# Kernel tuning notes

Hardware: AMD Instinct MI355X
Metric: run time of the kernel (lower is better)

Reference implementation:

```python
import jax, jax.numpy as jnp
import numpy as np

N, C, H, E = 4096, 512, 8, 131072
D = C // H
ALPHA = 0.5
EPS = 1e-5


def layer_norm(x, g, b):
    mu = jnp.mean(x, axis=-1, keepdims=True)
    var = jnp.mean((x - mu) ** 2, axis=-1, keepdims=True)
    return (x - mu) * jax.lax.rsqrt(var + EPS) * g + b


def setup_inputs() -> dict:
    key = jax.random.key(0)
    ks = jax.random.split(key, 20)
    s = 0.02
    return {
        "x": jax.random.normal(ks[0], (N, C), jnp.float32),
        "edge_index": jax.random.randint(ks[1], (2, E), 0, N, jnp.int32),
        "local_w": jax.random.normal(ks[2], (C, C), jnp.float32) * s,
        "local_b": jnp.zeros((C,), jnp.float32),
        "in_proj_w": jax.random.normal(ks[3], (3 * C, C), jnp.float32) * s,
        "in_proj_b": jnp.zeros((3 * C,), jnp.float32),
        "attn_out_w": jax.random.normal(ks[4], (C, C), jnp.float32) * s,
        "attn_out_b": jnp.zeros((C,), jnp.float32),
        "output_w": jax.random.normal(ks[5], (C, C), jnp.float32) * s,
        "output_b": jnp.zeros((C,), jnp.float32),
        "norm1_g": jnp.ones((C,), jnp.float32),
        "norm1_b": jnp.zeros((C,), jnp.float32),
        "norm2_g": jnp.ones((C,), jnp.float32),
        "norm2_b": jnp.zeros((C,), jnp.float32),
        "ffn_w1": jax.random.normal(ks[6], (2 * C, C), jnp.float32) * s,
        "ffn_b1": jnp.zeros((2 * C,), jnp.float32),
        "ffn_w2": jax.random.normal(ks[7], (C, 2 * C), jnp.float32) * s,
        "ffn_b2": jnp.zeros((C,), jnp.float32),
    }


def reference(x, edge_index, local_w, local_b, in_proj_w, in_proj_b,
              attn_out_w, attn_out_b, output_w, output_b,
              norm1_g, norm1_b, norm2_g, norm2_b,
              ffn_w1, ffn_b1, ffn_w2, ffn_b2):
    src, dst = edge_index[0], edge_index[1]

    # local branch: linear then scatter-mean over incoming edges
    local_h = x @ local_w.T + local_b                       # [N,C]
    summed = jax.ops.segment_sum(local_h[src], dst, num_segments=N)
    cnt = jax.ops.segment_sum(jnp.ones((E,), x.dtype), dst, num_segments=N)
    local_out = summed / jnp.maximum(cnt, 1.0)[:, None]

    # global branch: full self-attention over all nodes
    qkv = x @ in_proj_w.T + in_proj_b                       # [N,3C]
    q, k, v = jnp.split(qkv, 3, axis=-1)
    q = q.reshape(N, H, D)
    k = k.reshape(N, H, D)
    v = v.reshape(N, H, D)
    scores = jnp.einsum('nhd,mhd->hnm', q, k) / jnp.sqrt(jnp.asarray(D, x.dtype))
    attn = jax.nn.softmax(scores, axis=-1)                  # [H,N,N]
    ctx = jnp.einsum('hnm,mhd->nhd', attn, v).reshape(N, C)
    global_out = ctx @ attn_out_w.T + attn_out_b

    mixed = ALPHA * local_out + (1.0 - ALPHA) * global_out
    hidden = layer_norm(x + (mixed @ output_w.T + output_b), norm1_g, norm1_b)

    ff = jax.nn.gelu(hidden @ ffn_w1.T + ffn_b1, approximate=False) @ ffn_w2.T + ffn_b2
    return layer_norm(hidden + ff, norm2_g, norm2_b)
```

## Files before the change

kernel.cpp:

```cpp
#include <hip/hip_runtime.h>


#define N_NODES 4096
#define C_DIM   512
#define H_HEADS 8
#define D_HEAD  64
#define E_EDGES 131072

typedef unsigned short u16;
typedef unsigned int   u32;
typedef u16   u16x8  __attribute__((ext_vector_type(8)));
typedef __bf16 bf16x8 __attribute__((ext_vector_type(8)));
typedef float  f32x4  __attribute__((ext_vector_type(4)));
typedef u32    u32x4  __attribute__((ext_vector_type(4)));

__device__ __forceinline__ float b2f(u16 u) {
  unsigned int i = ((unsigned int)u) << 16;
  return __builtin_bit_cast(float, i);
}
__device__ __forceinline__ u16 f2b(float f) {
  unsigned int i = __builtin_bit_cast(unsigned int, f);
  i += 0x7fffu + ((i >> 16) & 1u);
  return (u16)(i >> 16);
}
__device__ __forceinline__ u32 cvtpk(float lo, float hi) {
  u32 r;
  asm("v_cvt_pk_bf16_f32 %0, %1, %2" : "=v"(r) : "v"(lo), "v"(hi));
  return r;
}
__device__ __forceinline__ void pl32swap(u32& x, u32& y) {
  asm("v_permlane32_swap_b32 %0, %1" : "+v"(x), "+v"(y));
}
__device__ __forceinline__ void pl16swap(u32& x, u32& y) {
  asm("v_permlane16_swap_b32 %0, %1" : "+v"(x), "+v"(y));
}
__device__ __forceinline__ void glds16(const u16* g, u16* l) {
  __builtin_amdgcn_global_load_lds(
      (const __attribute__((address_space(1))) void*)g,
      (__attribute__((address_space(3))) void*)l, 16, 0, 0);
}

struct CvtArgs {
  const float* src[7];
  u16* dst[7];
  int n[7];
  int* deg;
};

__global__ __launch_bounds__(256) void cvt_multi(CvtArgs a) {
  const int t = blockIdx.y;
  if (t == 7) {
    const int i = blockIdx.x * 256 + threadIdx.x;
    if (i < N_NODES) a.deg[i] = 0;
    return;
  }
  const int i = (blockIdx.x * 256 + threadIdx.x) * 8;
  if (i >= a.n[t]) return;
  const float* s = a.src[t] + i;
  f32x4 v0 = *(const f32x4*)s;
  f32x4 v1 = *(const f32x4*)(s + 4);
  u16x8 o;
  o[0]=f2b(v0[0]); o[1]=f2b(v0[1]); o[2]=f2b(v0[2]); o[3]=f2b(v0[3]);
  o[4]=f2b(v1[0]); o[5]=f2b(v1[1]); o[6]=f2b(v1[2]); o[7]=f2b(v1[3]);
  *(u16x8*)(a.dst[t] + i) = o;
}

template<int EPI>
__global__ __launch_bounds__(256) void gemm_bt(
    const u16* __restrict__ A, const u16* __restrict__ W,
    const float* __restrict__ bias, void* __restrict__ outp,
    int M, int Nout, int K,
    const float* __restrict__ mloc)
{
  const int tid  = threadIdx.x;
  const int lane = tid & 63, wave = tid >> 6;
  const int quad = lane >> 4, l16 = lane & 15;
  const int wm = wave >> 1, wn = wave & 1;
  const int bm = blockIdx.x, bnb = blockIdx.y;

  __shared__ __align__(16) u16 As[64][128];
  __shared__ __align__(16) u16 Ws[64][128];

  f32x4 acc[2][2] = {};

  const int lr4 = lane >> 4, gs = lane & 15;
  const int g8e = (gs ^ lr4) * 8;
  const int g8o = (gs ^ (4 + lr4)) * 8;
  const u16* aw[8];
#pragma unroll
  for (int c = 0; c < 4; ++c) {
    const int g8 = (c & 1) ? g8o : g8e;
    aw[c]     = A + (size_t)(bm  * 64 + wave * 16 + c * 4 + lr4) * K + g8;
    aw[4 + c] = W + (size_t)(bnb * 64 + wave * 16 + c * 4 + lr4) * K + g8;
  }

  for (int k0 = 0; k0 < K; k0 += 128) {
    __syncthreads();
#pragma unroll
    for (int c = 0; c < 4; ++c) {
      glds16(aw[c] + k0,     &As[wave * 16 + c * 4][0]);
      glds16(aw[4 + c] + k0, &Ws[wave * 16 + c * 4][0]);
    }
    __syncthreads();
#pragma unroll
    for (int ks = 0; ks < 4; ++ks) {
      const int slot = ((ks * 4 + quad) ^ (l16 & 7)) * 8;
      bf16x8 af[2], bf[2];
      af[0] = *(const bf16x8*)&As[wm * 32 +      l16][slot];
      af[1] = *(const bf16x8*)&As[wm * 32 + 16 + l16][slot];
      bf[0] = *(const bf16x8*)&Ws[wn * 32 +      l16][slot];
      bf[1] = *(const bf16x8*)&Ws[wn * 32 + 16 + l16][slot];
#pragma unroll
      for (int i = 0; i < 2; ++i)
#pragma unroll
        for (int j = 0; j < 2; ++j)
          acc[i][j] = __builtin_amdgcn_mfma_f32_16x16x32_bf16(af[i], bf[j], acc[i][j], 0, 0, 0);
    }
  }

#pragma unroll
  for (int i = 0; i < 2; ++i)
#pragma unroll
    for (int j = 0; j < 2; ++j) {
      const int col = bnb * 64 + wn * 32 + j * 16 + l16;
      const float bias_v = bias[col];
#pragma unroll
      for (int r = 0; r < 4; ++r) {
        const int row = bm * 64 + wm * 32 + i * 16 + quad * 4 + r;
        float v = acc[i][j][r] + bias_v;
        const size_t o = (size_t)row * Nout + col;
        if constexpr (EPI == 1) {
          ((float*)outp)[o] = v;
        } else if constexpr (EPI == 2) {
          float gl = 0.5f * v * (1.0f + erff(v * 0.70710678118654752f));
          ((u16*)outp)[o] = f2b(gl);
        } else {
          ((u16*)outp)[o] = f2b(0.5f * mloc[o] + 0.5f * v);
        }
      }
    }
}

__global__ __launch_bounds__(256) void gemm128(
    const u16* __restrict__ A, const u16* __restrict__ W,
    const float* __restrict__ bias0, const float* __restrict__ bias1,
    u16* __restrict__ out0, u16* __restrict__ out1,
    int M, int Nout, int K,
    const int* __restrict__ ei, int* __restrict__ deg)
{
  const int tid  = threadIdx.x;
  if (blockIdx.y == 16) {
#pragma unroll
    for (int i = 0; i < 16; ++i) {
      const int e = blockIdx.x * 4096 + i * 256 + tid;
      atomicAdd(&deg[ei[E_EDGES + e]], 1);
    }
    return;
  }
  const int lane = tid & 63, wave = tid >> 6;
  const int quad = lane >> 4, l16 = lane & 15;
  const int wm = wave >> 1, wn = wave & 1;
  const int bm = blockIdx.x, bnb = blockIdx.y;

  __shared__ __align__(16) u16 As[128][64];
  __shared__ __align__(16) u16 Ws[128][64];

  f32x4 acc[4][4] = {};

  const int lr = lane >> 3, gs = lane & 7;
  const int g8 = (gs ^ lr) * 8;
  const u16* ab = A + (size_t)(bm  * 128 + wave * 32 + lr) * K + g8;
  const u16* wb = W + (size_t)(bnb * 128 + wave * 32 + lr) * K + g8;

  for (int k0 = 0; k0 < K; k0 += 64) {
    __syncthreads();
#pragma unroll
    for (int c = 0; c < 4; ++c) {
      glds16(ab + (size_t)(c * 8) * K + k0, &As[wave * 32 + c * 8][0]);
      glds16(wb + (size_t)(c * 8) * K + k0, &Ws[wave * 32 + c * 8][0]);
    }
    __syncthreads();
#pragma unroll
    for (int ks = 0; ks < 2; ++ks) {
      const int slot = ((ks * 4 + quad) ^ (l16 & 7)) * 8;
      bf16x8 af[4], bf[4];
#pragma unroll
      for (int am = 0; am < 4; ++am)
        af[am] = *(const bf16x8*)&As[wm * 64 + am * 16 + l16][slot];
#pragma unroll
      for (int bn = 0; bn < 4; ++bn)
        bf[bn] = *(const bf16x8*)&Ws[wn * 64 + bn * 16 + l16][slot];
#pragma unroll
      for (int am = 0; am < 4; ++am)
#pragma unroll
        for (int bn = 0; bn < 4; ++bn)
          acc[am][bn] = __builtin_amdgcn_mfma_f32_16x16x32_bf16(af[am], bf[bn], acc[am][bn], 0, 0, 0);
    }
  }

#pragma unroll
  for (int am = 0; am < 4; ++am)
#pragma unroll
    for (int bn = 0; bn < 4; ++bn) {
      const int col = bnb * 128 + wn * 64 + bn * 16 + l16;
      const float bias_v = (col < 512) ? bias0[col] : bias1[col - 512];
#pragma unroll
      for (int r = 0; r < 4; ++r) {
        const int row = bm * 128 + wm * 64 + am * 16 + quad * 4 + r;
        float v = acc[am][bn][r] + bias_v;
        if (col < 512) out0[(size_t)row * 512 + col] = f2b(v);
        else           out1[(size_t)row * 1536 + (col - 512)] = f2b(v);
      }
    }
}

__global__ __launch_bounds__(256) void scan_vtrans(
    const int* __restrict__ deg, int* __restrict__ off, int* __restrict__ cursor,
    const u16* __restrict__ qkv, u16* __restrict__ vt)
{
  if (blockIdx.x == 512) {
    __shared__ int part[256];
    const int t = threadIdx.x;
    int v[16];
    int s = 0;
#pragma unroll
    for (int i = 0; i < 16; ++i) { v[i] = deg[t * 16 + i]; s += v[i]; }
    part[t] = s;
    __syncthreads();
    for (int d = 1; d < 256; d <<= 1) {
      int val = (t >= d) ? part[t - d] : 0;
      __syncthreads();
      if (t >= d) part[t] += val;
      __syncthreads();
    }
    int prefix = (t == 0) ? 0 : part[t - 1];
#pragma unroll
    for (int i = 0; i < 16; ++i) {
      off[t * 16 + i] = prefix;
      cursor[t * 16 + i] = prefix;
      prefix += v[i];
    }
    if (t == 255) off[4096] = prefix;
    return;
  }
  __shared__ __align__(16) u16 T[64][64];
  const int tid = threadIdx.x;
  const int h = blockIdx.x >> 6, mt = blockIdx.x & 63;
  const int m0 = mt * 64;
  const int c  = tid & 7;
  const int mr = tid >> 3;
#pragma unroll
  for (int half = 0; half < 2; ++half) {
    const int m = mr + half * 32;
    const u16x8 v = *(const u16x8*)(qkv + (size_t)(m0 + m) * 1536 + 1024 + h * 64 + c * 8);
    *(u16x8*)&T[m][((c ^ (m >> 3)) * 8)] = v;
  }
  __syncthreads();
#pragma unroll
  for (int half = 0; half < 2; ++half) {
    const int q = tid + half * 256;
    const int d = q >> 3, mc = q & 7;
    u16x8 w;
#pragma unroll
    for (int e = 0; e < 8; ++e)
      w[e] = T[mc * 8 + e][(((d >> 3) ^ mc) * 8) + (d & 7)];
    *(u16x8*)(vt + (size_t)(h * 64 + d) * N_NODES + m0 + mc * 8) = w;
  }
}

template<int SPLITS>
__global__ __launch_bounds__(256) void attn_kernel(
    const u16* __restrict__ qkv, const u16* __restrict__ vt,
    u16* __restrict__ opart, float* __restrict__ lpart,
    const int* __restrict__ ei, int* __restrict__ cursor, int* __restrict__ csr)
{
  const int tid = threadIdx.x, wave = tid >> 6, lane = tid & 63;
  const int split = blockIdx.z;
  if (split == SPLITS) {
    const int sblk = blockIdx.y * 32 + blockIdx.x;
#pragma unroll
    for (int i = 0; i < 2; ++i) {
      const int e = sblk * 512 + i * 256 + tid;
      const int s = ei[e];
      const int d = ei[E_EDGES + e];
      const int p = atomicAdd(&cursor[d], 1);
      csr[p] = s;
    }
    return;
  }
  const int quad = lane >> 4, l16 = lane & 15;
  const int h = blockIdx.x & 7;
  const int tile = (blockIdx.x >> 3) + (blockIdx.y << 2);

  __shared__ __align__(16) u16 Ks[2][64][64];
  __shared__ __align__(16) u16 Vts[2][64][64];

  const float QSCALE = 0.18033688011112042f;
  bf16x8 aq[2][2];
#pragma unroll
  for (int mb = 0; mb < 2; ++mb) {
    const int qrow = tile * 128 + wave * 32 + mb * 16 + l16;
    const u16* qp = qkv + (size_t)qrow * 1536 + h * 64 + quad * 8;
    u16x8 q0 = *(const u16x8*)qp;
    u16x8 q1 = *(const u16x8*)(qp + 32);
    u16x8 s0, s1;
#pragma unroll
    for (int i = 0; i < 8; ++i) {
      s0[i] = f2b(b2f(q0[i]) * QSCALE);
      s1[i] = f2b(b2f(q1[i]) * QSCALE);
    }
    aq[mb][0] = __builtin_bit_cast(bf16x8, s0);
    aq[mb][1] = __builtin_bit_cast(bf16x8, s1);
  }

  u16x8 ones_u;
#pragma unroll
  for (int i = 0; i < 8; ++i) ones_u[i] = 0x3F80;
  const bf16x8 vone = __builtin_bit_cast(bf16x8, ones_u);

  f32x4 O[2][4] = {};
  f32x4 lacc[2] = {};

  const int lr = lane >> 3, gs = lane & 7;
  const int g8 = (gs ^ lr) * 8;
  const int R0 = wave * 16 + lr;

  const u16* kp = qkv + (size_t)R0 * 1536 + 512 + h * 64 + g8;
  const u16* vp = vt + (size_t)(h * 64 + R0) * N_NODES + g8;

  const int mt0 = split * (64 / SPLITS), mt1 = (split + 1) * (64 / SPLITS);

  {
    const size_t ko = (size_t)mt0 * 64 * 1536;
    glds16(kp + ko,            &Ks[0][wave * 16][0]);
    glds16(kp + ko + 8 * 1536, &Ks[0][wave * 16 + 8][0]);
    glds16(vp + mt0 * 64,               &Vts[0][wave * 16][0]);
    glds16(vp + mt0 * 64 + 8 * N_NODES, &Vts[0][wave * 16 + 8][0]);
  }

  for (int mt = mt0; mt < mt1; ++mt) {
    const int cur = (mt - mt0) & 1;
    asm volatile("s_waitcnt vmcnt(0)" ::: "memory");
    __builtin_amdgcn_s_barrier();
    __builtin_amdgcn_sched_barrier(0);
    if (mt + 1 < mt1) {
      const size_t ko = (size_t)(mt + 1) * 64 * 1536;
      glds16(kp + ko,            &Ks[cur ^ 1][wave * 16][0]);
      glds16(kp + ko + 8 * 1536, &Ks[cur ^ 1][wave * 16 + 8][0]);
      glds16(vp + (mt + 1) * 64,               &Vts[cur ^ 1][wave * 16][0]);
      glds16(vp + (mt + 1) * 64 + 8 * N_NODES, &Vts[cur ^ 1][wave * 16 + 8][0]);
    }

    f32x4 st[2][4] = {};
    __builtin_amdgcn_s_setprio(1);
#pragma unroll
    for (int ks = 0; ks < 2; ++ks) {
      const int slot = ((ks * 4 + quad) ^ (l16 & 7)) * 8;
      bf16x8 af[4];
#pragma unroll
      for (int jn = 0; jn < 4; ++jn)
        af[jn] = *(const bf16x8*)&Ks[cur][jn * 16 + l16][slot];
#pragma unroll
      for (int mb = 0; mb < 2; ++mb)
#pragma unroll
        for (int jn = 0; jn < 4; ++jn)
          st[mb][jn] = __builtin_amdgcn_mfma_f32_16x16x32_bf16(af[jn], aq[mb][ks], st[mb][jn], 0, 0, 0);
    }
    __builtin_amdgcn_s_setprio(0);

    bf16x8 pa[2][2];
#pragma unroll
    for (int mb = 0; mb < 2; ++mb) {
      u32 pk[4][2];
#pragma unroll
      for (int jn = 0; jn < 4; ++jn) {
        float p0 = __builtin_amdgcn_exp2f(st[mb][jn][0]);
        float p1 = __builtin_amdgcn_exp2f(st[mb][jn][1]);
        float p2 = __builtin_amdgcn_exp2f(st[mb][jn][2]);
        float p3 = __builtin_amdgcn_exp2f(st[mb][jn][3]);
        pk[jn][0] = cvtpk(p0, p1);
        pk[jn][1] = cvtpk(p2, p3);
      }
#pragma unroll
      for (int ks = 0; ks < 2; ++ks) {
        u32 x0 = pk[2 * ks][0], y0 = pk[2 * ks + 1][0];
        u32 x1 = pk[2 * ks][1], y1 = pk[2 * ks + 1][1];
        pl32swap(x0, y0); pl16swap(x0, y0);
        pl32swap(x1, y1); pl16swap(x1, y1);
        u32x4 av;
        av[0] = x0; av[1] = x1; av[2] = y0; av[3] = y1;
        pa[mb][ks] = __builtin_bit_cast(bf16x8, av);
      }
    }

    __builtin_amdgcn_s_setprio(1);
#pragma unroll
    for (int ks = 0; ks < 2; ++ks) {
      const int slot = ((ks * 4 + quad) ^ (l16 & 7)) * 8;
      bf16x8 bv[4];
#pragma unroll
      for (int jd = 0; jd < 4; ++jd)
        bv[jd] = *(const bf16x8*)&Vts[cur][jd * 16 + l16][slot];
#pragma unroll
      for (int mb = 0; mb < 2; ++mb) {
#pragma unroll
        for (int jd = 0; jd < 4; ++jd)
          O[mb][jd] = __builtin_amdgcn_mfma_f32_16x16x32_bf16(pa[mb][ks], bv[jd], O[mb][jd], 0, 0, 0);
        lacc[mb] = __builtin_amdgcn_mfma_f32_16x16x32_bf16(pa[mb][ks], vone, lacc[mb], 0, 0, 0);
      }
    }
    __builtin_amdgcn_s_setprio(0);
  }

#pragma unroll
  for (int mb = 0; mb < 2; ++mb) {
#pragma unroll
    for (int r = 0; r < 4; ++r) {
      const int row = tile * 128 + wave * 32 + mb * 16 + quad * 4 + r;
      u16* orow = opart + ((size_t)split * N_NODES + row) * C_DIM + h * 64;
#pragma unroll
      for (int jd = 0; jd < 4; ++jd)
        orow[jd * 16 + l16] = f2b(O[mb][jd][r]);
      if (l16 == 0)
        lpart[((size_t)split * N_NODES + row) * H_HEADS + h] = lacc[mb][r];
    }
  }
}

template<int SPLITS>
__global__ __launch_bounds__(256) void combine_gather(
    const u16* __restrict__ opart, const float* __restrict__ lpart,
    u16* __restrict__ ctx,
    const int* __restrict__ off, const int* __restrict__ csr,
    const u16* __restrict__ lh, float* __restrict__ lo)
{
  if (blockIdx.y == 0) {
    const int wave = threadIdx.x >> 6, lane = threadIdx.x & 63;
    const int n = blockIdx.x * 4 + wave;
    const int j0 = off[n], j1 = off[n + 1];
    float acc[8] = {};
    int j = j0;
    for (; j + 4 <= j1; j += 4) {
      const int s0 = csr[j], s1 = csr[j + 1], s2 = csr[j + 2], s3 = csr[j + 3];
      const u16x8 v0 = *(const u16x8*)(lh + (size_t)s0 * C_DIM + lane * 8);
      const u16x8 v1 = *(const u16x8*)(lh + (size_t)s1 * C_DIM + lane * 8);
      const u16x8 v2 = *(const u16x8*)(lh + (size_t)s2 * C_DIM + lane * 8);
      const u16x8 v3 = *(const u16x8*)(lh + (size_t)s3 * C_DIM + lane * 8);
#pragma unroll
      for (int i = 0; i < 8; ++i)
        acc[i] += (b2f(v0[i]) + b2f(v1[i])) + (b2f(v2[i]) + b2f(v3[i]));
    }
    for (; j < j1; ++j) {
      const int s = csr[j];
      const u16x8 v = *(const u16x8*)(lh + (size_t)s * C_DIM + lane * 8);
#pragma unroll
      for (int i = 0; i < 8; ++i) acc[i] += b2f(v[i]);
    }
    const float inv = 1.0f / fmaxf((float)(j1 - j0), 1.0f);
    f32x4 o0, o1;
#pragma unroll
    for (int i = 0; i < 4; ++i) { o0[i] = acc[i] * inv; o1[i] = acc[4 + i] * inv; }
    float* op = lo + (size_t)n * C_DIM + lane * 8;
    *(f32x4*)op = o0;
    *(f32x4*)(op + 4) = o1;
    return;
  }
  const size_t base = (size_t)(blockIdx.x * 256 + threadIdx.x) * 8;
  const int row = (int)(base >> 9);
  const int h = (int)((base & 511) >> 6);
  float l = 0.0f;
#pragma unroll
  for (int s = 0; s < SPLITS; ++s)
    l += lpart[(size_t)s * N_NODES * H_HEADS + (size_t)row * H_HEADS + h];
  const float inv = 1.0f / l;
  float o[8] = {};
#pragma unroll
  for (int s = 0; s < SPLITS; ++s) {
    const u16x8 p = *(const u16x8*)(opart + (size_t)s * N_NODES * C_DIM + base);
#pragma unroll
    for (int i = 0; i < 8; ++i) o[i] += b2f(p[i]);
  }
  u16x8 ob;
#pragma unroll
  for (int i = 0; i < 8; ++i) ob[i] = f2b(o[i] * inv);
  *(u16x8*)(ctx + base) = ob;
}

__global__ __launch_bounds__(256) void ln1_kernel(
    const float* __restrict__ x, const float* __restrict__ pr,
    const float* __restrict__ g, const float* __restrict__ b,
    u16* __restrict__ hb, float* __restrict__ hf)
{
  const int wave = threadIdx.x >> 6, lane = threadIdx.x & 63;
  const int row = blockIdx.x * 4 + wave;
  const int c0 = lane * 8;
  const size_t base = (size_t)row * C_DIM + c0;
  f32x4 x0 = *(const f32x4*)(x + base);
  f32x4 x1 = *(const f32x4*)(x + base + 4);
  f32x4 p0 = *(const f32x4*)(pr + base);
  f32x4 p1 = *(const f32x4*)(pr + base + 4);
  float v[8];
#pragma unroll
  for (int i = 0; i < 4; ++i) { v[i] = x0[i] + p0[i]; v[4 + i] = x1[i] + p1[i]; }
  float sum = 0, sq = 0;
#pragma unroll
  for (int i = 0; i < 8; ++i) { sum += v[i]; sq += v[i] * v[i]; }
  for (int off = 1; off < 64; off <<= 1) { sum += __shfl_xor(sum, off); sq += __shfl_xor(sq, off); }
  const float mean = sum * (1.0f / C_DIM);
  const float var  = sq * (1.0f / C_DIM) - mean * mean;
  const float rstd = rsqrtf(var + 1e-5f);
  f32x4 g0 = *(const f32x4*)(g + c0), g1 = *(const f32x4*)(g + c0 + 4);
  f32x4 b0 = *(const f32x4*)(b + c0), b1 = *(const f32x4*)(b + c0 + 4);
  u16x8 ob; f32x4 h0, h1;
#pragma unroll
  for (int i = 0; i < 4; ++i) {
    float hv0 = (v[i]     - mean) * rstd * g0[i] + b0[i];
    float hv1 = (v[4 + i] - mean) * rstd * g1[i] + b1[i];
    h0[i] = hv0; h1[i] = hv1;
    ob[i] = f2b(hv0); ob[4 + i] = f2b(hv1);
  }
  *(u16x8*)(hb + base) = ob;
  *(f32x4*)(hf + base) = h0;
  *(f32x4*)(hf + base + 4) = h1;
}

__global__ __launch_bounds__(256) void ln2_kernel(
    const float* __restrict__ a, const float* __restrict__ c,
    const float* __restrict__ g, const float* __restrict__ b,
    float* __restrict__ out)
{
  const int wave = threadIdx.x >> 6, lane = threadIdx.x & 63;
  const int row = blockIdx.x * 4 + wave;
  const int c0 = lane * 8;
  const size_t base = (size_t)row * C_DIM + c0;
  f32x4 a0 = *(const f32x4*)(a + base), a1 = *(const f32x4*)(a + base + 4);
  f32x4 c0v = *(const f32x4*)(c + base), c1v = *(const f32x4*)(c + base + 4);
  float v[8];
#pragma unroll
  for (int i = 0; i < 4; ++i) { v[i] = a0[i] + c0v[i]; v[4 + i] = a1[i] + c1v[i]; }
  float sum = 0, sq = 0;
#pragma unroll
  for (int i = 0; i < 8; ++i) { sum += v[i]; sq += v[i] * v[i]; }
  for (int off = 1; off < 64; off <<= 1) { sum += __shfl_xor(sum, off); sq += __shfl_xor(sq, off); }
  const float mean = sum * (1.0f / C_DIM);
  const float var  = sq * (1.0f / C_DIM) - mean * mean;
  const float rstd = rsqrtf(var + 1e-5f);
  f32x4 g0 = *(const f32x4*)(g + c0), g1 = *(const f32x4*)(g + c0 + 4);
  f32x4 b0 = *(const f32x4*)(b + c0), b1 = *(const f32x4*)(b + c0 + 4);
  f32x4 h0, h1;
#pragma unroll
  for (int i = 0; i < 4; ++i) {
    h0[i] = (v[i]     - mean) * rstd * g0[i] + b0[i];
    h1[i] = (v[4 + i] - mean) * rstd * g1[i] + b1[i];
  }
  *(f32x4*)(out + base) = h0;
  *(f32x4*)(out + base + 4) = h1;
}

extern "C" void kernel_launch(void* const* d_in, const int* in_sizes, int n_in,
                              void* d_out, int out_size, void* d_ws, size_t ws_size,
                              hipStream_t stream) {
  const float* x          = (const float*)d_in[0];
  const int*   ei         = (const int*)d_in[1];
  const float* local_w    = (const float*)d_in[2];
  const float* local_b    = (const float*)d_in[3];
  const float* in_proj_w  = (const float*)d_in[4];
  const float* in_proj_b  = (const float*)d_in[5];
  const float* attn_out_w = (const float*)d_in[6];
  const float* attn_out_b = (const float*)d_in[7];
  const float* output_w   = (const float*)d_in[8];
  const float* output_b   = (const float*)d_in[9];
  const float* n1g = (const float*)d_in[10];
  const float* n1b = (const float*)d_in[11];
  const float* n2g = (const float*)d_in[12];
  const float* n2b = (const float*)d_in[13];
  const float* ffn_w1 = (const float*)d_in[14];
  const float* ffn_b1 = (const float*)d_in[15];
  const float* ffn_w2 = (const float*)d_in[16];
  const float* ffn_b2 = (const float*)d_in[17];
  float* out = (float*)d_out;

  char* ws = (char*)d_ws;
  size_t o = 0;
  float* local_out = (float*)(ws + o); o += (size_t)N_NODES * C_DIM * 4;
  int* deg    = (int*)(ws + o); o += (N_NODES) * 4;
  int* off    = (int*)(ws + o); o += (N_NODES + 16) * 4;
  int* cursor = (int*)(ws + o); o += (N_NODES) * 4;
  int* csr    = (int*)(ws + o); o += (size_t)E_EDGES * 4;
  u16* xb   = (u16*)(ws + o); o += (size_t)N_NODES * C_DIM * 2;
  u16* wbLQ = (u16*)(ws + o); o += (size_t)4 * C_DIM * C_DIM * 2;
  u16* wbA  = (u16*)(ws + o); o += (size_t)C_DIM * C_DIM * 2;
  u16* wbO  = (u16*)(ws + o); o += (size_t)C_DIM * C_DIM * 2;
  u16* wbF1 = (u16*)(ws + o); o += (size_t)2 * C_DIM * C_DIM * 2;
  u16* wbF2 = (u16*)(ws + o); o += (size_t)2 * C_DIM * C_DIM * 2;
  u16* local_h   = (u16*)(ws + o); o += (size_t)N_NODES * C_DIM * 2;
  u16* qkvb      = (u16*)(ws + o); o += (size_t)N_NODES * 3 * C_DIM * 2;
  u16* ctxb      = (u16*)(ws + o); o += (size_t)N_NODES * C_DIM * 2;
  u16* mixed     = (u16*)(ws + o); o += (size_t)N_NODES * C_DIM * 2;
  u16* hidden_bf = (u16*)(ws + o); o += (size_t)N_NODES * C_DIM * 2;
  float* hidden_f = (float*)(ws + o); o += (size_t)N_NODES * C_DIM * 4;
  u16* ff1       = (u16*)(ws + o); o += (size_t)N_NODES * 2 * C_DIM * 2;
  float* proj  = (float*)qkvb;
  float* ff2   = (float*)local_out;
  u16*   vt    = xb;
  u16* opart4 = (u16*)(ws + o);
  float* lpart4 = (float*)(ws + o + (size_t)4 * N_NODES * C_DIM * 2);
  const size_t need4 = o + (size_t)4 * N_NODES * C_DIM * 2 + (size_t)4 * N_NODES * H_HEADS * 4;
  const bool use4 = (ws_size >= need4);
  u16* opart2 = (u16*)hidden_bf;
  float* lpart2 = (float*)(opart2 + (size_t)2 * N_NODES * C_DIM);

  CvtArgs ca;
  ca.src[0] = x;          ca.dst[0] = xb;   ca.n[0] = N_NODES * C_DIM;
  ca.src[1] = local_w;    ca.dst[1] = wbLQ;                  ca.n[1] = C_DIM * C_DIM;
  ca.src[2] = in_proj_w;  ca.dst[2] = wbLQ + C_DIM * C_DIM;  ca.n[2] = 3 * C_DIM * C_DIM;
  ca.src[3] = attn_out_w; ca.dst[3] = wbA;  ca.n[3] = C_DIM * C_DIM;
  ca.src[4] = output_w;   ca.dst[4] = wbO;  ca.n[4] = C_DIM * C_DIM;
  ca.src[5] = ffn_w1;     ca.dst[5] = wbF1; ca.n[5] = 2 * C_DIM * C_DIM;
  ca.src[6] = ffn_w2;     ca.dst[6] = wbF2; ca.n[6] = 2 * C_DIM * C_DIM;
  ca.deg = deg;
  cvt_multi<<<dim3(N_NODES * C_DIM / 2048, 8), 256, 0, stream>>>(ca);

  gemm128<<<dim3(32, 17), 256, 0, stream>>>(xb, wbLQ, local_b, in_proj_b,
      local_h, qkvb, N_NODES, 4 * C_DIM, C_DIM, ei, deg);

  scan_vtrans<<<513, 256, 0, stream>>>(deg, off, cursor, qkvb, vt);

  if (use4) {
    attn_kernel<4><<<dim3(32, 8, 5), 256, 0, stream>>>(qkvb, vt, opart4, lpart4,
        ei, cursor, csr);
    combine_gather<4><<<dim3(1024, 2), 256, 0, stream>>>(opart4, lpart4, ctxb,
        off, csr, local_h, local_out);
  } else {
    attn_kernel<2><<<dim3(32, 8, 3), 256, 0, stream>>>(qkvb, vt, opart2, lpart2,
        ei, cursor, csr);
    combine_gather<2><<<dim3(1024, 2), 256, 0, stream>>>(opart2, lpart2, ctxb,
        off, csr, local_h, local_out);
  }

  gemm_bt<3><<<dim3(64, 8), 256, 0, stream>>>(ctxb, wbA, attn_out_b, mixed,
      N_NODES, C_DIM, C_DIM, local_out);

  gemm_bt<1><<<dim3(64, 8), 256, 0, stream>>>(mixed, wbO, output_b, proj,
      N_NODES, C_DIM, C_DIM, nullptr);
  ln1_kernel<<<N_NODES / 4, 256, 0, stream>>>(x, proj, n1g, n1b, hidden_bf, hidden_f);

  gemm_bt<2><<<dim3(64, 16), 256, 0, stream>>>(hidden_bf, wbF1, ffn_b1, ff1,
      N_NODES, 2 * C_DIM, C_DIM, nullptr);
  gemm_bt<1><<<dim3(64, 8), 256, 0, stream>>>(ff1, wbF2, ffn_b2, ff2,
      N_NODES, C_DIM, 2 * C_DIM, nullptr);
  ln2_kernel<<<N_NODES / 4, 256, 0, stream>>>(hidden_f, ff2, n2g, n2b, out);
}
```

Baseline: 243.6 us.

## Reschedule graph-aggregation stages to overlap with attention and GEMM kernels

Moves the side work of the graph branch one stage earlier so that each piece hides behind larger kernels. The degree count now runs inside the conversion kernel after a memset. The prefix scan runs as an extra block of the QKV GEMM, and CSR filling runs alongside the V transpose. The neighbour gather-mean runs as extra blocks in the attention kernel instead of in the combine kernel. The aim is to remove serial tail work from the combine step and shorten the critical path, at the cost of heavier blocks sharing the attention grid and one extra memset launch.

```diff
diff --git a/kernel.cpp b/kernel.cpp
--- a/kernel.cpp
+++ b/kernel.cpp
@@ -45,13 +45,16 @@
   u16* dst[7];
   int n[7];
   int* deg;
+  const int* ei;
 };
 
 __global__ __launch_bounds__(256) void cvt_multi(CvtArgs a) {
   const int t = blockIdx.y;
   if (t == 7) {
-    const int i = blockIdx.x * 256 + threadIdx.x;
-    if (i < N_NODES) a.deg[i] = 0;
+    if (blockIdx.x < 512) {
+      const int e = blockIdx.x * 256 + threadIdx.x;
+      atomicAdd(&a.deg[a.ei[E_EDGES + e]], 1);
+    }
     return;
   }
   const int i = (blockIdx.x * 256 + threadIdx.x) * 8;
@@ -146,81 +149,13 @@
     const float* __restrict__ bias0, const float* __restrict__ bias1,
     u16* __restrict__ out0, u16* __restrict__ out1,
     int M, int Nout, int K,
-    const int* __restrict__ ei, int* __restrict__ deg)
+    const int* __restrict__ deg, int* __restrict__ off, int* __restrict__ cursor)
 {
   const int tid  = threadIdx.x;
   if (blockIdx.y == 16) {
-#pragma unroll
-    for (int i = 0; i < 16; ++i) {
-      const int e = blockIdx.x * 4096 + i * 256 + tid;
-      atomicAdd(&deg[ei[E_EDGES + e]], 1);
-    }
-    return;
-  }
-  const int lane = tid & 63, wave = tid >> 6;
-  const int quad = lane >> 4, l16 = lane & 15;
-  const int wm = wave >> 1, wn = wave & 1;
-  const int bm = blockIdx.x, bnb = blockIdx.y;
-
-  __shared__ __align__(16) u16 As[128][64];
-  __shared__ __align__(16) u16 Ws[128][64];
-
-  f32x4 acc[4][4] = {};
-
-  const int lr = lane >> 3, gs = lane & 7;
-  const int g8 = (gs ^ lr) * 8;
-  const u16* ab = A + (size_t)(bm  * 128 + wave * 32 + lr) * K + g8;
-  const u16* wb = W + (size_t)(bnb * 128 + wave * 32 + lr) * K + g8;
-
-  for (int k0 = 0; k0 < K; k0 += 64) {
-    __syncthreads();
-#pragma unroll
-    for (int c = 0; c < 4; ++c) {
-      glds16(ab + (size_t)(c * 8) * K + k0, &As[wave * 32 + c * 8][0]);
-      glds16(wb + (size_t)(c * 8) * K + k0, &Ws[wave * 32 + c * 8][0]);
-    }
-    __syncthreads();
-#pragma unroll
-    for (int ks = 0; ks < 2; ++ks) {
-      const int slot = ((ks * 4 + quad) ^ (l16 & 7)) * 8;
-      bf16x8 af[4], bf[4];
-#pragma unroll
-      for (int am = 0; am < 4; ++am)
-        af[am] = *(const bf16x8*)&As[wm * 64 + am * 16 + l16][slot];
-#pragma unroll
-      for (int bn = 0; bn < 4; ++bn)
-        bf[bn] = *(const bf16x8*)&Ws[wn * 64 + bn * 16 + l16][slot];
-#pragma unroll
-      for (int am = 0; am < 4; ++am)
-#pragma unroll
-        for (int bn = 0; bn < 4; ++bn)
-          acc[am][bn] = __builtin_amdgcn_mfma_f32_16x16x32_bf16(af[am], bf[bn], acc[am][bn], 0, 0, 0);
-    }
-  }
-
-#pragma unroll
-  for (int am = 0; am < 4; ++am)
-#pragma unroll
-    for (int bn = 0; bn < 4; ++bn) {
-      const int col = bnb * 128 + wn * 64 + bn * 16 + l16;
-      const float bias_v = (col < 512) ? bias0[col] : bias1[col - 512];
-#pragma unroll
-      for (int r = 0; r < 4; ++r) {
-        const int row = bm * 128 + wm * 64 + am * 16 + quad * 4 + r;
-        float v = acc[am][bn][r] + bias_v;
-        if (col < 512) out0[(size_t)row * 512 + col] = f2b(v);
-        else           out1[(size_t)row * 1536 + (col - 512)] = f2b(v);
-      }
-    }
-}
-
-__global__ __launch_bounds__(256) void scan_vtrans(
-    const int* __restrict__ deg, int* __restrict__ off, int* __restrict__ cursor,
-    const u16* __restrict__ qkv, u16* __restrict__ vt)
-{
-  if (blockIdx.x == 512) {
+    if (blockIdx.x != 0) return;
     __shared__ int part[256];
-    const int t = threadIdx.x;
+    const int t = tid;
     int v[16];
     int s = 0;
 #pragma unroll
@@ -243,41 +178,70 @@
     if (t == 255) off[4096] = prefix;
     return;
   }
-  __shared__ __align__(16) u16 T[64][64];
-  const int tid = threadIdx.x;
-  const int h = blockIdx.x >> 6, mt = blockIdx.x & 63;
-  const int m0 = mt * 64;
-  const int c  = tid & 7;
-  const int mr = tid >> 3;
-#pragma unroll
-  for (int half = 0; half < 2; ++half) {
-    const int m = mr + half * 32;
-    const u16x8 v = *(const u16x8*)(qkv + (size_t)(m0 + m) * 1536 + 1024 + h * 64 + c * 8);
-    *(u16x8*)&T[m][((c ^ (m >> 3)) * 8)] = v;
-  }
-  __syncthreads();
-#pragma unroll
-  for (int half = 0; half < 2; ++half) {
-    const int q = tid + half * 256;
-    const int d = q >> 3, mc = q & 7;
-    u16x8 w;
-#pragma unroll
-    for (int e = 0; e < 8; ++e)
-      w[e] = T[mc * 8 + e][(((d >> 3) ^ mc) * 8) + (d & 7)];
-    *(u16x8*)(vt + (size_t)(h * 64 + d) * N_NODES + m0 + mc * 8) = w;
-  }
-}
-
-template<int SPLITS>
-__global__ __launch_bounds__(256) void attn_kernel(
-    const u16* __restrict__ qkv, const u16* __restrict__ vt,
-    u16* __restrict__ opart, float* __restrict__ lpart,
+  const int lane = tid & 63, wave = tid >> 6;
+  const int quad = lane >> 4, l16 = lane & 15;
+  const int wm = wave >> 1, wn = wave & 1;
+  const int bm = blockIdx.x, bnb = blockIdx.y;
+
+  __shared__ __align__(16) u16 As[128][64];
+  __shared__ __align__(16) u16 Ws[128][64];
+
+  f32x4 acc[4][4] = {};
+
+  const int lr = lane >> 3, gs = lane & 7;
+  const int g8 = (gs ^ lr) * 8;
+  const u16* ab = A + (size_t)(bm  * 128 + wave * 32 + lr) * K + g8;
+  const u16* wb = W + (size_t)(bnb * 128 + wave * 32 + lr) * K + g8;
+
+  for (int k0 = 0; k0 < K; k0 += 64) {
+    __syncthreads();
+#pragma unroll
+    for (int c = 0; c < 4; ++c) {
+      glds16(ab + (size_t)(c * 8) * K + k0, &As[wave * 32 + c * 8][0]);
+      glds16(wb + (size_t)(c * 8) * K + k0, &Ws[wave * 32 + c * 8][0]);
+    }
+    __syncthreads();
+#pragma unroll
+    for (int ks = 0; ks < 2; ++ks) {
+      const int slot = ((ks * 4 + quad) ^ (l16 & 7)) * 8;
+      bf16x8 af[4], bf[4];
+#pragma unroll
+      for (int am = 0; am < 4; ++am)
+        af[am] = *(const bf16x8*)&As[wm * 64 + am * 16 + l16][slot];
+#pragma unroll
+      for (int bn = 0; bn < 4; ++bn)
+        bf[bn] = *(const bf16x8*)&Ws[wn * 64 + bn * 16 + l16][slot];
+#pragma unroll
+      for (int am = 0; am < 4; ++am)
+#pragma unroll
+        for (int bn = 0; bn < 4; ++bn)
+          acc[am][bn] = __builtin_amdgcn_mfma_f32_16x16x32_bf16(af[am], bf[bn], acc[am][bn], 0, 0, 0);
+    }
+  }
+
+#pragma unroll
+  for (int am = 0; am < 4; ++am)
+#pragma unroll
+    for (int bn = 0; bn < 4; ++bn) {
+      const int col = bnb * 128 + wn * 64 + bn * 16 + l16;
+      const float bias_v = (col < 512) ? bias0[col] : bias1[col - 512];
+#pragma unroll
+      for (int r = 0; r < 4; ++r) {
+        const int row = bm * 128 + wm * 64 + am * 16 + quad * 4 + r;
+        float v = acc[am][bn][r] + bias_v;
+        if (col < 512) out0[(size_t)row * 512 + col] = f2b(v);
+        else           out1[(size_t)row * 1536 + (col - 512)] = f2b(v);
+      }
+    }
+}
+
+__global__ __launch_bounds__(256) void vtrans_fill(
+    const u16* __restrict__ qkv, u16* __restrict__ vt,
     const int* __restrict__ ei, int* __restrict__ cursor, int* __restrict__ csr)
 {
-  const int tid = threadIdx.x, wave = tid >> 6, lane = tid & 63;
-  const int split = blockIdx.z;
-  if (split == SPLITS) {
-    const int sblk = blockIdx.y * 32 + blockIdx.x;
+  const int tid = threadIdx.x;
+  if (blockIdx.x >= 512) {
+    const int sblk = blockIdx.x - 512;
 #pragma unroll
     for (int i = 0; i < 2; ++i) {
       const int e = sblk * 512 + i * 256 + tid;
@@ -286,6 +250,70 @@
       const int p = atomicAdd(&cursor[d], 1);
       csr[p] = s;
     }
+    return;
+  }
+  __shared__ __align__(16) u16 T[64][64];
+  const int h = blockIdx.x >> 6, mt = blockIdx.x & 63;
+  const int m0 = mt * 64;
+  const int c  = tid & 7;
+  const int mr = tid >> 3;
+#pragma unroll
+  for (int half = 0; half < 2; ++half) {
+    const int m = mr + half * 32;
+    const u16x8 v = *(const u16x8*)(qkv + (size_t)(m0 + m) * 1536 + 1024 + h * 64 + c * 8);
+    *(u16x8*)&T[m][((c ^ (m >> 3)) * 8)] = v;
+  }
+  __syncthreads();
+#pragma unroll
+  for (int half = 0; half < 2; ++half) {
+    const int q = tid + half * 256;
+    const int d = q >> 3, mc = q & 7;
+    u16x8 w;
+#pragma unroll
+    for (int e = 0; e < 8; ++e)
+      w[e] = T[mc * 8 + e][(((d >> 3) ^ mc) * 8) + (d & 7)];
+    *(u16x8*)(vt + (size_t)(h * 64 + d) * N_NODES + m0 + mc * 8) = w;
+  }
+}
+
+template<int SPLITS>
+__global__ __launch_bounds__(256) void attn_kernel(
+    const u16* __restrict__ qkv, const u16* __restrict__ vt,
+    u16* __restrict__ opart, float* __restrict__ lpart,
+    const int* __restrict__ off, const int* __restrict__ csr,
+    const u16* __restrict__ lh, float* __restrict__ lo)
+{
+  const int tid = threadIdx.x, wave = tid >> 6, lane = tid & 63;
+  const int split = blockIdx.z;
+  if (split >= SPLITS) {
+    const int gblk = (split - SPLITS) * 256 + blockIdx.y * 32 + blockIdx.x;
+    const int n = gblk * 4 + wave;
+    const int j0 = off[n], j1 = off[n + 1];
+    float acc[8] = {};
+    int j = j0;
+    for (; j + 4 <= j1; j += 4) {
+      const int s0 = csr[j], s1 = csr[j + 1], s2 = csr[j + 2], s3 = csr[j + 3];
+      const u16x8 v0 = *(const u16x8*)(lh + (size_t)s0 * C_DIM + lane * 8);
+      const u16x8 v1 = *(const u16x8*)(lh + (size_t)s1 * C_DIM + lane * 8);
+      const u16x8 v2 = *(const u16x8*)(lh + (size_t)s2 * C_DIM + lane * 8);
+      const u16x8 v3 = *(const u16x8*)(lh + (size_t)s3 * C_DIM + lane * 8);
+#pragma unroll
+      for (int i = 0; i < 8; ++i)
+        acc[i] += (b2f(v0[i]) + b2f(v1[i])) + (b2f(v2[i]) + b2f(v3[i]));
+    }
+    for (; j < j1; ++j) {
+      const int s = csr[j];
+      const u16x8 v = *(const u16x8*)(lh + (size_t)s * C_DIM + lane * 8);
+#pragma unroll
+      for (int i = 0; i < 8; ++i) acc[i] += b2f(v[i]);
+    }
+    const float inv = 1.0f / fmaxf((float)(j1 - j0), 1.0f);
+    f32x4 o0, o1;
+#pragma unroll
+    for (int i = 0; i < 4; ++i) { o0[i] = acc[i] * inv; o1[i] = acc[4 + i] * inv; }
+    float* op = lo + (size_t)n * C_DIM + lane * 8;
+    *(f32x4*)op = o0;
+    *(f32x4*)(op + 4) = o1;
     return;
   }
   const int quad = lane >> 4, l16 = lane & 15;
@@ -428,43 +456,10 @@
 }
 
 template<int SPLITS>
-__global__ __launch_bounds__(256) void combine_gather(
+__global__ __launch_bounds__(256) void combine_kernel(
     const u16* __restrict__ opart, const float* __restrict__ lpart,
-    u16* __restrict__ ctx,
-    const int* __restrict__ off, const int* __restrict__ csr,
-    const u16* __restrict__ lh, float* __restrict__ lo)
+    u16* __restrict__ ctx)
 {
-  if (blockIdx.y == 0) {
-    const int wave = threadIdx.x >> 6, lane = threadIdx.x & 63;
-    const int n = blockIdx.x * 4 + wave;
-    const int j0 = off[n], j1 = off[n + 1];
-    float acc[8] = {};
-    int j = j0;
-    for (; j + 4 <= j1; j += 4) {
-      const int s0 = csr[j], s1 = csr[j + 1], s2 = csr[j + 2], s3 = csr[j + 3];
-      const u16x8 v0 = *(const u16x8*)(lh + (size_t)s0 * C_DIM + lane * 8);
-      const u16x8 v1 = *(const u16x8*)(lh + (size_t)s1 * C_DIM + lane * 8);
-      const u16x8 v2 = *(const u16x8*)(lh + (size_t)s2 * C_DIM + lane * 8);
-      const u16x8 v3 = *(const u16x8*)(lh + (size_t)s3 * C_DIM + lane * 8);
-#pragma unroll
-      for (int i = 0; i < 8; ++i)
-        acc[i] += (b2f(v0[i]) + b2f(v1[i])) + (b2f(v2[i]) + b2f(v3[i]));
-    }
-    for (; j < j1; ++j) {
-      const int s = csr[j];
-      const u16x8 v = *(const u16x8*)(lh + (size_t)s * C_DIM + lane * 8);
-#pragma unroll
-      for (int i = 0; i < 8; ++i) acc[i] += b2f(v[i]);
-    }
-    const float inv = 1.0f / fmaxf((float)(j1 - j0), 1.0f);
-    f32x4 o0, o1;
-#pragma unroll
-    for (int i = 0; i < 4; ++i) { o0[i] = acc[i] * inv; o1[i] = acc[4 + i] * inv; }
-    float* op = lo + (size_t)n * C_DIM + lane * 8;
-    *(f32x4*)op = o0;
-    *(f32x4*)(op + 4) = o1;
-    return;
-  }
   const size_t base = (size_t)(blockIdx.x * 256 + threadIdx.x) * 8;
   const int row = (int)(base >> 9);
   const int h = (int)((base & 511) >> 6);
@@ -610,6 +605,8 @@
   u16* opart2 = (u16*)hidden_bf;
   float* lpart2 = (float*)(opart2 + (size_t)2 * N_NODES * C_DIM);
 
+  hipMemsetAsync(deg, 0, N_NODES * sizeof(int), stream);
+
   CvtArgs ca;
   ca.src[0] = x;          ca.dst[0] = xb;   ca.n[0] = N_NODES * C_DIM;
   ca.src[1] = local_w;    ca.dst[1] = wbLQ;                  ca.n[1] = C_DIM * C_DIM;
@@ -619,23 +616,22 @@
   ca.src[5] = ffn_w1;     ca.dst[5] = wbF1; ca.n[5] = 2 * C_DIM * C_DIM;
   ca.src[6] = ffn_w2;     ca.dst[6] = wbF2; ca.n[6] = 2 * C_DIM * C_DIM;
   ca.deg = deg;
+  ca.ei = ei;
   cvt_multi<<<dim3(N_NODES * C_DIM / 2048, 8), 256, 0, stream>>>(ca);
 
   gemm128<<<dim3(32, 17), 256, 0, stream>>>(xb, wbLQ, local_b, in_proj_b,
-      local_h, qkvb, N_NODES, 4 * C_DIM, C_DIM, ei, deg);
-
-  scan_vtrans<<<513, 256, 0, stream>>>(deg, off, cursor, qkvb, vt);
+      local_h, qkvb, N_NODES, 4 * C_DIM, C_DIM, deg, off, cursor);
+
+  vtrans_fill<<<768, 256, 0, stream>>>(qkvb, vt, ei, cursor, csr);
 
   if (use4) {
-    attn_kernel<4><<<dim3(32, 8, 5), 256, 0, stream>>>(qkvb, vt, opart4, lpart4,
-        ei, cursor, csr);
-    combine_gather<4><<<dim3(1024, 2), 256, 0, stream>>>(opart4, lpart4, ctxb,
+    attn_kernel<4><<<dim3(32, 8, 8), 256, 0, stream>>>(qkvb, vt, opart4, lpart4,
         off, csr, local_h, local_out);
+    combine_kernel<4><<<1024, 256, 0, stream>>>(opart4, lpart4, ctxb);
   } else {
-    attn_kernel<2><<<dim3(32, 8, 3), 256, 0, stream>>>(qkvb, vt, opart2, lpart2,
-        ei, cursor, csr);
-    combine_gather<2><<<dim3(1024, 2), 256, 0, stream>>>(opart2, lpart2, ctxb,
+    attn_kernel<2><<<dim3(32, 8, 6), 256, 0, stream>>>(qkvb, vt, opart2, lpart2,
         off, csr, local_h, local_out);
+    combine_kernel<2><<<1024, 256, 0, stream>>>(opart2, lpart2, ctxb);
   }
 
   gemm_bt<3><<<dim3(64, 8), 256, 0, stream>>>(ctxb, wbA, attn_out_b, mixed,
```

After: 249.0 us. 2.2% more time.
